# Optimization experiments

Measured on AMD Instinct MI355X. Metric: run time of the kernel, lower is better.

## Reference

```python
import jax, jax.numpy as jnp
import numpy as np

NUM_HEADS = 12
ROPE_THETA = 100.0

def _rotate_half(x):
    x1 = x[..., ::2]
    x2 = x[..., 1::2]
    return jnp.stack((-x2, x1), axis=-1).reshape(x.shape)

def _apply_rope(x, cos, sin):
    return x * cos + _rotate_half(x) * sin

def _rope_cos_sin(h, w, head_dim, theta):
    quarter = head_dim // 4  # head_dim=64 -> 16 freq bands
    inv_freq = 1.0 / theta ** (jnp.arange(quarter, dtype=jnp.float32) / max(quarter, 1))
    y = jnp.repeat(jnp.arange(h, dtype=jnp.float32), w)   # [h*w]
    xc = jnp.tile(jnp.arange(w, dtype=jnp.float32), h)    # [h*w]
    y_freqs = y[:, None] * inv_freq[None, :]               # [N, quarter]
    x_freqs = xc[:, None] * inv_freq[None, :]
    y_ang = jnp.repeat(y_freqs, 2, axis=-1)                # [N, half]
    x_ang = jnp.repeat(x_freqs, 2, axis=-1)
    ang = jnp.concatenate([y_ang, x_ang], axis=-1)         # [N, head_dim]
    return jnp.cos(ang)[None, None], jnp.sin(ang)[None, None]  # [1,1,N,hd]

def setup_inputs() -> dict:
    key = jax.random.key(0)
    ks = jax.random.split(key, 8)
    B, S, D = 8, 1025, 768
    s = 0.02
    return {
        "x": jax.random.normal(ks[0], (B, S, D), jnp.float32),
        "q_w": jax.random.normal(ks[1], (D, D), jnp.float32) * s,
        "q_b": jax.random.normal(ks[2], (D,), jnp.float32) * s,
        "k_w": jax.random.normal(ks[3], (D, D), jnp.float32) * s,
        "v_w": jax.random.normal(ks[4], (D, D), jnp.float32) * s,
        "v_b": jax.random.normal(ks[5], (D,), jnp.float32) * s,
        "o_w": jax.random.normal(ks[6], (D, D), jnp.float32) * s,
        "o_b": jax.random.normal(ks[7], (D,), jnp.float32) * s,
        "h": 32,
        "w": 32,
        "num_prefix_tokens": 1,
    }

def reference(x, q_w, q_b, k_w, v_w, v_b, o_w, o_b, h, w, num_prefix_tokens):
    B, S, D = x.shape
    H = NUM_HEADS
    hd = D // H
    scale = hd ** -0.5
    p = num_prefix_tokens

    def proj(W, b):
        y = jnp.einsum('bsd,ed->bse', x, W)
        if b is not None:
            y = y + b
        return y.reshape(B, S, H, hd).transpose(0, 2, 1, 3)  # [B,H,S,hd]

    q = proj(q_w, q_b)
    k = proj(k_w, None)
    v = proj(v_w, v_b)

    cos, sin = _rope_cos_sin(h, w, hd, ROPE_THETA)
    q = jnp.concatenate([q[:, :, :p], _apply_rope(q[:, :, p:], cos, sin)], axis=2)
    k = jnp.concatenate([k[:, :, :p], _apply_rope(k[:, :, p:], cos, sin)], axis=2)

    attn = jnp.einsum('bhqd,bhkd->bhqk', q * scale, k)
    attn = jax.nn.softmax(attn, axis=-1)
    out = jnp.einsum('bhqk,bhkd->bhqd', attn, v)
    out = out.transpose(0, 2, 1, 3).reshape(B, S, D)
    return jnp.einsum('bsd,ed->bse', out, o_w) + o_b
```

## Files before the change

### kernel.cpp

```cpp
#include <hip/hip_runtime.h>

typedef unsigned short u16;
typedef unsigned int   u32;
typedef __attribute__((ext_vector_type(4))) short s4;
typedef __attribute__((ext_vector_type(8))) short s8;
typedef __attribute__((ext_vector_type(4))) float f4;
typedef __attribute__((ext_vector_type(16))) float f16v;

#define NB   8
#define SEQ  1025
#define DIM  768
#define NH   12
#define HD   64
#define BPAD 1056
#define MPAD 8448
#define MV   8200
#define SQP  1056
#define SKP  1088
#define NG16 68
#define NQKV 2304
#define BHT  96
#define QSCALE 0.1803368801111204f

__device__ __forceinline__ u16 f2bf(float f) {
  u32 u = __builtin_bit_cast(u32, f);
  u += 0x7fffu + ((u >> 16) & 1u);
  return (u16)(u >> 16);
}
__device__ __forceinline__ float bf2f(u16 h) {
  return __builtin_bit_cast(float, ((u32)h) << 16);
}
__device__ __forceinline__ float exp2f_(float x) {
#if __has_builtin(__builtin_amdgcn_exp2f)
  return __builtin_amdgcn_exp2f(x);
#else
  return exp2f(x);
#endif
}
__device__ __forceinline__ u32 cvtpk(float a, float b) {
  u32 r;
  asm("v_cvt_pk_bf16_f32 %0, %1, %2" : "=v"(r) : "v"(a), "v"(b));
  return r;
}

typedef const __attribute__((address_space(1))) void cas1v;
typedef __attribute__((address_space(3))) void as3v;
__device__ __forceinline__ void gload16(const void* g, void* l) {
  __builtin_amdgcn_global_load_lds((cas1v*)g, (as3v*)l, 16, 0, 0);
}

#define MFMA16(a, b, c) __builtin_amdgcn_mfma_f32_16x16x32_bf16(a, b, c, 0, 0, 0)
#define MFMA32(a, b, c) __builtin_amdgcn_mfma_f32_32x32x16_bf16(a, b, c, 0, 0, 0)
#define BAR() __builtin_amdgcn_s_barrier()

__global__ void conv_x(const float* __restrict__ x, u16* __restrict__ xb) {
  int i = blockIdx.x * 256 + threadIdx.x;
  int e = i * 4;
  int row = e / DIM, col = e - row * DIM;
  int b = row / BPAD, s = row - b * BPAD;
  s4 o;
  if (s < SEQ) {
    float4 v = *(const float4*)(x + ((size_t)(b * SEQ + s)) * DIM + col);
    o[0] = (short)f2bf(v.x); o[1] = (short)f2bf(v.y);
    o[2] = (short)f2bf(v.z); o[3] = (short)f2bf(v.w);
  } else {
    o = (s4){0, 0, 0, 0};
  }
  *(s4*)(xb + e) = o;
}

__global__ void conv_w(const float* __restrict__ qw, const float* __restrict__ kw,
                       const float* __restrict__ vw, const float* __restrict__ ow,
                       const float* __restrict__ qb, const float* __restrict__ vb,
                       u16* __restrict__ wqkv, u16* __restrict__ wo, float* __restrict__ biasq,
                       float2* __restrict__ rt) {
  int i = blockIdx.x * 256 + threadIdx.x;
  wqkv[i]           = f2bf(qw[i]);
  wqkv[i + 589824]  = f2bf(kw[i]);
  wqkv[i + 1179648] = f2bf(vw[i]);
  wo[i]             = f2bf(ow[i]);
  if (i < NQKV) biasq[i] = (i < 768) ? qb[i] : (i < 1536 ? 0.f : vb[i - 1536]);
  if (i < SEQ * 32) {
    int s = i >> 5, jj = i & 31;
    float cs = 1.f, sn = 0.f;
    if (s > 0) {
      int tok = s - 1;
      int pos = (jj < 16) ? (tok >> 5) : (tok & 31);
      int f = jj & 15;
      float ang = (float)pos * __expf((float)f * -0.28782313662425572f);
      __sincosf(ang, &sn, &cs);
    }
    rt[i] = make_float2(cs, sn);
  }
}

__global__ __launch_bounds__(512, 2) void gemm_qkv(const u16* __restrict__ A, const u16* __restrict__ Bm,
                                                   const float* __restrict__ bias,
                                                   u16* __restrict__ Ql, u16* __restrict__ Kl,
                                                   u16* __restrict__ Vp, const float2* __restrict__ rt) {
  __shared__ u16 smem[73728];
  const int K = DIM;
  int tid = threadIdx.x;
  int lane = tid & 63, wave = tid >> 6;
  int g = lane >> 4, c16 = lane & 15;
  int wm = wave >> 1, wn = wave & 1;
  int nwg = gridDim.x, orig = blockIdx.x;
  int qd = nwg >> 3, rm = nwg & 7, xcd = orig & 7;
  int wgid = (xcd < rm ? xcd * (qd + 1) : rm * (qd + 1) + (xcd - rm) * qd) + (orig >> 3);
  int m0 = (wgid / 18) * 256, n0 = (wgid % 18) * 128;

  f4 acc[4][4] = {};

  int lr = lane >> 3;
  int lc = ((lane & 7) ^ lr) * 8;
  const u16* As0 = A  + (size_t)(m0 + wave * 8 + lr) * K + lc;
  const u16* Bs0 = Bm + (size_t)(n0 + wave * 8 + lr) * K + lc;

  auto stageA3 = [&](int sb, int ko) {
    u16* base = smem + sb * 24576 + wave * 512;
    gload16(As0 + ko,           base);
    gload16(As0 + 64 * K + ko,  base + 4096);
    gload16(As0 + 128 * K + ko, base + 8192);
  };
  auto stageB3 = [&](int sb, int ko) {
    u16* baseA = smem + sb * 24576 + wave * 512;
    u16* baseB = smem + sb * 24576 + 16384 + wave * 512;
    gload16(As0 + 192 * K + ko, baseA + 12288);
    gload16(Bs0 + ko,           baseB);
    gload16(Bs0 + 64 * K + ko,  baseB + 4096);
  };

  int rsw = (c16 & 7) << 3;
  int colk0 = (g * 8) ^ rsw;
  int colk1 = (g * 8 + 32) ^ rsw;

  stageA3(0, 0);  stageB3(0, 0);
  stageA3(1, 64); stageB3(1, 64);
  asm volatile("s_waitcnt vmcnt(6)" ::: "memory");
  BAR();

#pragma unroll 3
  for (int kt = 0; kt < 12; ++kt) {
    const u16* bp = smem + (kt % 3) * 24576;
    int sb = (kt + 2) % 3, ko = (kt + 2) * 64;
    bool st = kt < 10;
    s8 bfr[4][2], afr[2][2];
#pragma unroll
    for (int n = 0; n < 4; n++) {
      int rb = wn * 64 + n * 16 + c16;
      bfr[n][0] = *(const s8*)(bp + 16384 + rb * 64 + colk0);
      bfr[n][1] = *(const s8*)(bp + 16384 + rb * 64 + colk1);
    }
#pragma unroll
    for (int m = 0; m < 2; m++) {
      int ra = wm * 64 + m * 16 + c16;
      afr[m][0] = *(const s8*)(bp + ra * 64 + colk0);
      afr[m][1] = *(const s8*)(bp + ra * 64 + colk1);
    }
    if (st) stageA3(sb, ko);
    BAR();
    asm volatile("s_waitcnt lgkmcnt(0)" ::: "memory");
    __builtin_amdgcn_s_setprio(1);
#pragma unroll
    for (int m = 0; m < 2; m++)
#pragma unroll
      for (int n = 0; n < 4; n++) {
        acc[m][n] = MFMA16(afr[m][0], bfr[n][0], acc[m][n]);
        acc[m][n] = MFMA16(afr[m][1], bfr[n][1], acc[m][n]);
      }
    __builtin_amdgcn_s_setprio(0);
    BAR();
    s8 af2[2][2];
#pragma unroll
    for (int m = 0; m < 2; m++) {
      int ra = wm * 64 + (m + 2) * 16 + c16;
      af2[m][0] = *(const s8*)(bp + ra * 64 + colk0);
      af2[m][1] = *(const s8*)(bp + ra * 64 + colk1);
    }
    if (st) stageB3(sb, ko);
    BAR();
    asm volatile("s_waitcnt lgkmcnt(0)" ::: "memory");
    __builtin_amdgcn_s_setprio(1);
#pragma unroll
    for (int m = 0; m < 2; m++)
#pragma unroll
      for (int n = 0; n < 4; n++) {
        acc[m + 2][n] = MFMA16(af2[m][0], bfr[n][0], acc[m + 2][n]);
        acc[m + 2][n] = MFMA16(af2[m][1], bfr[n][1], acc[m + 2][n]);
      }
    __builtin_amdgcn_s_setprio(0);
    if (kt < 10)       asm volatile("s_waitcnt vmcnt(6)" ::: "memory");
    else if (kt == 10) asm volatile("s_waitcnt vmcnt(0)" ::: "memory");
    BAR();
  }

  __syncthreads();
  u16 (*ct)[130] = (u16(*)[130])smem;
  int part = (n0 >= 1536) ? 2 : (n0 >= 768 ? 1 : 0);
  float qs = (part == 0) ? QSCALE : 1.0f;
#pragma unroll
  for (int j = 0; j < 4; j++) {
    int col = wn * 64 + j * 16 + c16;
    float bv = bias[n0 + col];
    int jj = (col & 63) >> 1;
    int odd = col & 1;
#pragma unroll
    for (int i = 0; i < 4; i++) {
      int rowb = wm * 64 + i * 16 + g * 4;
#pragma unroll
      for (int r = 0; r < 4; r++) {
        float v = acc[i][j][r] + bv;
        u16 o;
        if (part < 2) {
          float vp = __shfl_xor(v, 1);
          int m = m0 + rowb + r;
          int s = m % BPAD;
          float2 t = rt[(s < SEQ ? s : SEQ - 1) * 32 + jj];
          float rv = odd ? (v * t.x + vp * t.y) : (v * t.x - vp * t.y);
          o = f2bf(rv * qs);
        } else {
          o = f2bf(v);
        }
        ct[rowb + r][col] = o;
      }
    }
  }
  __syncthreads();
  if (part < 2) {
    u16* dstB = (part == 0) ? Ql : Kl;
    int stride = (part == 0) ? SQP : SKP;
#pragma unroll
    for (int p = 0; p < 8; p++) {
      int task = p * 512 + tid;
      int row = task >> 4, cg = (task & 15) * 8;
      int m = m0 + row, b = m / BPAD, s = m - b * BPAD;
      int n = n0 + cg;
      int hq = (n >> 6) - part * NH;
      s8 v = *(const s8*)&ct[row][cg];
      *(s8*)(dstB + ((size_t)((b * NH + hq) * stride + s)) * HD + (n & 63)) = v;
    }
  } else {
#pragma unroll
    for (int p = 0; p < 4; p++) {
      int task = p * 512 + tid;
      int col = task & 127, rg = task >> 7;
      int mb = m0 + rg * 16, b = mb / BPAD, sb2 = mb - b * BPAD;
      int g16 = sb2 >> 4;
      int n = n0 + col;
      int hq = (n >> 6) - 2 * NH;
      s8 o0, o1;
#pragma unroll
      for (int k = 0; k < 16; k++) {
        int mp = (k & 3) | (((k >> 3) & 1) << 2) | (((k >> 2) & 1) << 3);
        u16 val = ct[rg * 16 + k][col];
        if (mp < 8) o0[mp] = (short)val; else o1[mp - 8] = (short)val;
      }
      u16* dst = Vp + ((size_t)((b * NH + hq) * NG16 + g16) * HD + (n & 63)) * 16;
      *(s8*)dst = o0;
      *(s8*)(dst + 8) = o1;
    }
  }
}

__global__ __launch_bounds__(256) void gemm_o(const u16* __restrict__ A, const u16* __restrict__ Bm,
                                              float* __restrict__ Cf, const float* __restrict__ bias,
                                              int N, int K, int Mvalid, int nnt) {
  __shared__ u16 smem[16384];
  int tid = threadIdx.x;
  int lane = tid & 63, wave = tid >> 6;
  int g = lane >> 4, c16 = lane & 15;
  int nwg = gridDim.x, orig = blockIdx.x;
  int qd = nwg >> 3, rm = nwg & 7, xcd = orig & 7;
  int wgid = (xcd < rm ? xcd * (qd + 1) : rm * (qd + 1) + (xcd - rm) * qd) + (orig >> 3);
  int m0 = (wgid / nnt) * 128, n0 = (wgid % nnt) * 128;
  int wm = wave >> 1, wn = wave & 1;
  f4 acc[4][4] = {};

  int ldrow = wave * 16 + (lane >> 2);
  int ldk = ((lane & 3) ^ ((ldrow >> 1) & 3)) * 8;
  const u16* Asrc = A + (size_t)(m0 + ldrow) * K + ldk;
  const u16* Bsrc = Bm + (size_t)(n0 + ldrow) * K + ldk;

  auto stage = [&](int buf, int k0) {
    u16* aw = smem + buf * 4096 + wave * 512;
    u16* bw = smem + 8192 + buf * 4096 + wave * 512;
    gload16(Asrc + k0, aw);
    gload16(Asrc + 64 * K + k0, aw + 2048);
    gload16(Bsrc + k0, bw);
    gload16(Bsrc + 64 * K + k0, bw + 2048);
  };

  stage(0, 0);
  __syncthreads();
  int nk = K >> 5;
  int kx = (g ^ ((c16 >> 1) & 3)) * 8;
  for (int t = 0; t < nk; t++) {
    int buf = t & 1;
    if (t + 1 < nk) stage(buf ^ 1, (t + 1) << 5);
    s8 af[4], bf[4];
#pragma unroll
    for (int i = 0; i < 4; i++) {
      af[i] = *(const s8*)(smem + buf * 4096 + (wm * 64 + i * 16 + c16) * 32 + kx);
      bf[i] = *(const s8*)(smem + 8192 + buf * 4096 + (wn * 64 + i * 16 + c16) * 32 + kx);
    }
    __builtin_amdgcn_s_setprio(1);
#pragma unroll
    for (int i = 0; i < 4; i++)
#pragma unroll
      for (int j = 0; j < 4; j++)
        acc[i][j] = MFMA16(af[i], bf[j], acc[i][j]);
    __builtin_amdgcn_s_setprio(0);
    __syncthreads();
  }

#pragma unroll
  for (int i = 0; i < 4; i++)
#pragma unroll
    for (int j = 0; j < 4; j++) {
      int n = n0 + wn * 64 + j * 16 + c16;
      float bv = bias[n];
#pragma unroll
      for (int r = 0; r < 4; r++) {
        int m = m0 + wm * 64 + i * 16 + g * 4 + r;
        if (m < Mvalid) Cf[(size_t)m * N + n] = acc[i][j][r] + bv;
      }
    }
}

__global__ __launch_bounds__(256) void attn_k(const u16* __restrict__ Q, const u16* __restrict__ K,
                                              const u16* __restrict__ Vp, u16* __restrict__ Ao) {
  __shared__ u16 lds[2][2][64 * 64];
  int bh = blockIdx.x;
  int tid = threadIdx.x;
  int wave = tid >> 6, lane = tid & 63;
  int q32 = lane & 31, h = lane >> 5;
  int b = bh / NH, hh = bh % NH;
  int qb = blockIdx.y * 128 + wave * 32;
  if (qb > SEQ - 32) qb = SEQ - 32;
  const u16* Qb = Q + (size_t)bh * SQP * HD;
  const u16* Kb = K + (size_t)bh * SKP * HD;
  const u16* Vb = Vp + (size_t)bh * NG16 * 1024;

  s8 qf[4];
#pragma unroll
  for (int t = 0; t < 4; t++)
    qf[t] = *(const s8*)(Qb + (size_t)(qb + q32) * HD + 16 * t + 8 * h);

  f16v o0 = {}, o1 = {};
  float mrun = -3e38f, lrun = 0.f;
  int swz = (q32 & 7) << 4;

  auto stage = [&](int buf, int c) {
#pragma unroll
    for (int i = 0; i < 2; i++) {
      int sb = i * 4096 + tid * 16;
      int row = sb >> 7;
      int ch = (sb >> 4) & 7;
      int so = (ch ^ (row & 7)) * 8;
      u16* kd = &lds[buf][0][i * 2048 + wave * 512];
      u16* vd = &lds[buf][1][i * 2048 + wave * 512];
      gload16(Kb + (size_t)(c * 64 + row) * HD + so, kd);
      gload16(Vb + c * 4096 + i * 2048 + tid * 8, vd);
    }
  };

  stage(0, 0);
  __syncthreads();

  for (int c = 0; c < 17; c++) {
    int buf = c & 1;
    if (c < 16) stage(buf ^ 1, c + 1);
    const char* Ks = (const char*)&lds[buf][0][0];
    const char* Vs = (const char*)&lds[buf][1][0];

    f16v st0 = {}, st1 = {};
    __builtin_amdgcn_s_setprio(1);
#pragma unroll
    for (int t = 0; t < 4; t++) {
      int off = (32 * t + 16 * h) ^ swz;
      s8 a0 = *(const s8*)(Ks + q32 * 128 + off);
      s8 a1 = *(const s8*)(Ks + (32 + q32) * 128 + off);
      st0 = MFMA32(a0, qf[t], st0);
      st1 = MFMA32(a1, qf[t], st1);
    }
    __builtin_amdgcn_s_setprio(0);

    s8 vf0[4], vf1[4];
#pragma unroll
    for (int s = 0; s < 4; s++) {
      vf0[s] = *(const s8*)(Vs + 2048 * s + 32 * q32 + 16 * h);
      vf1[s] = *(const s8*)(Vs + 2048 * s + 1024 + 32 * q32 + 16 * h);
    }

    if (c == 16) {
      st0[0] = h ? -3e38f : st0[0];
#pragma unroll
      for (int r = 1; r < 16; r++) st0[r] = -3e38f;
#pragma unroll
      for (int r = 0; r < 16; r++) st1[r] = -3e38f;
    }

    float mx[8];
#pragma unroll
    for (int r = 0; r < 8; r++)
      mx[r] = fmaxf(fmaxf(st0[r], st0[r + 8]), fmaxf(st1[r], st1[r + 8]));
#pragma unroll
    for (int w = 4; w >= 1; w >>= 1)
#pragma unroll
      for (int r = 0; r < w; r++) mx[r] = fmaxf(mx[r], mx[r + w]);
    float pmax = fmaxf(mx[0], __shfl_xor(mx[0], 32));

    if (!__all(pmax <= mrun + 11.5f)) {
      float mnew = fmaxf(mrun, pmax);
      float cf = exp2f_(mrun - mnew);
      lrun *= cf;
      mrun = mnew;
#pragma unroll
      for (int r = 0; r < 16; r++) {
        float c2 = __shfl(cf, (r & 3) + 8 * (r >> 2) + 4 * h);
        o0[r] *= c2;
        o1[r] *= c2;
      }
    }

    float sm[8];
#pragma unroll
    for (int r = 0; r < 16; r++) {
      st0[r] = exp2f_(st0[r] - mrun);
      st1[r] = exp2f_(st1[r] - mrun);
    }
#pragma unroll
    for (int r = 0; r < 8; r++) sm[r] = (st0[r] + st0[r + 8]) + (st1[r] + st1[r + 8]);
#pragma unroll
    for (int w = 4; w >= 1; w >>= 1)
#pragma unroll
      for (int r = 0; r < w; r++) sm[r] += sm[r + w];
    lrun += sm[0] + __shfl_xor(sm[0], 32);

    __builtin_amdgcn_s_setprio(1);
#pragma unroll
    for (int s = 0; s < 4; s++) {
      union { s8 v; u32 w[4]; } pa;
#pragma unroll
      for (int i = 0; i < 4; i++) {
        float plo = (s < 2) ? st0[8 * (s & 1) + 2 * i]     : st1[8 * (s & 1) + 2 * i];
        float phi = (s < 2) ? st0[8 * (s & 1) + 2 * i + 1] : st1[8 * (s & 1) + 2 * i + 1];
        pa.w[i] = cvtpk(plo, phi);
      }
      o0 = MFMA32(pa.v, vf0[s], o0);
      o1 = MFMA32(pa.v, vf1[s], o1);
    }
    __builtin_amdgcn_s_setprio(0);
    __syncthreads();
  }

  float rl = 1.0f / lrun;
#pragma unroll
  for (int r = 0; r < 16; r++) {
    int cr = (r & 3) + 8 * (r >> 2) + 4 * h;
    float sc = __shfl(rl, cr);
    u16* dst = Ao + (size_t)(b * SEQ + qb + cr) * DIM + hh * HD;
    dst[q32]      = f2bf(o0[r] * sc);
    dst[32 + q32] = f2bf(o1[r] * sc);
  }
}

extern "C" void kernel_launch(void* const* d_in, const int* in_sizes, int n_in,
                              void* d_out, int out_size, void* d_ws, size_t ws_size,
                              hipStream_t stream) {
  const float* x  = (const float*)d_in[0];
  const float* qw = (const float*)d_in[1];
  const float* qb = (const float*)d_in[2];
  const float* kw = (const float*)d_in[3];
  const float* vw = (const float*)d_in[4];
  const float* vb = (const float*)d_in[5];
  const float* ow = (const float*)d_in[6];
  const float* ob = (const float*)d_in[7];
  float* out = (float*)d_out;

  char* ws = (char*)d_ws;
  u16*    xb   = (u16*)(ws);
  u16*    wqkv = (u16*)(ws + 12976128);
  u16*    wo   = (u16*)(ws + 16515072);
  float*  bq   = (float*)(ws + 17694720);
  float2* rt   = (float2*)(ws + 17703936);
  u16*    Ql   = (u16*)(ws + 17966336);
  u16*    Kl   = (u16*)(ws + 30942464);
  u16*    Vp   = (u16*)(ws + 44311808);
  u16*    Ao   = xb;

  conv_x<<<6336, 256, 0, stream>>>(x, xb);
  conv_w<<<2304, 256, 0, stream>>>(qw, kw, vw, ow, qb, vb, wqkv, wo, bq, rt);
  gemm_qkv<<<594, 512, 0, stream>>>(xb, wqkv, bq, Ql, Kl, Vp, rt);
  attn_k<<<dim3(96, 9), 256, 0, stream>>>(Ql, Kl, Vp, Ao);
  gemm_o<<<390, 256, 0, stream>>>(Ao, wo, out, ob, DIM, DIM, MV, 6);
}
```

Baseline: 161.4 us.

## Enlarge QKV GEMM tile to 256x256 with double-buffered LDS and 2x4 waves

The fused QKV projection GEMM now uses 256x256 output tiles instead of 256x128. Each of 8 waves computes 128x64, and K tiles are double-buffered instead of triple-buffered, which halves the grid to 297 blocks at one block per CU. The larger tile is meant to raise operand reuse and cut global and LDS traffic per FLOP. In exchange, 297 blocks on 256 CUs leaves a ragged tail wave, occupancy drops, and there is less load-latency hiding.

```diff
diff --git a/kernel.cpp b/kernel.cpp
--- a/kernel.cpp
+++ b/kernel.cpp
@@ -52,6 +52,7 @@
 #define MFMA16(a, b, c) __builtin_amdgcn_mfma_f32_16x16x32_bf16(a, b, c, 0, 0, 0)
 #define MFMA32(a, b, c) __builtin_amdgcn_mfma_f32_32x32x16_bf16(a, b, c, 0, 0, 0)
 #define BAR() __builtin_amdgcn_s_barrier()
+#define LGKM0() do { asm volatile("s_waitcnt lgkmcnt(0)" ::: "memory"); __builtin_amdgcn_sched_barrier(0); } while (0)
 
 __global__ void conv_x(const float* __restrict__ x, u16* __restrict__ xb) {
   int i = blockIdx.x * 256 + threadIdx.x;
@@ -94,108 +95,143 @@
   }
 }
 
-__global__ __launch_bounds__(512, 2) void gemm_qkv(const u16* __restrict__ A, const u16* __restrict__ Bm,
+__global__ __launch_bounds__(512, 1) void gemm_qkv(const u16* __restrict__ A, const u16* __restrict__ Bm,
                                                    const float* __restrict__ bias,
                                                    u16* __restrict__ Ql, u16* __restrict__ Kl,
                                                    u16* __restrict__ Vp, const float2* __restrict__ rt) {
-  __shared__ u16 smem[73728];
+  __shared__ u16 smem[66560];
   const int K = DIM;
   int tid = threadIdx.x;
   int lane = tid & 63, wave = tid >> 6;
   int g = lane >> 4, c16 = lane & 15;
-  int wm = wave >> 1, wn = wave & 1;
+  int wm = wave >> 2, wn = wave & 3;
   int nwg = gridDim.x, orig = blockIdx.x;
   int qd = nwg >> 3, rm = nwg & 7, xcd = orig & 7;
   int wgid = (xcd < rm ? xcd * (qd + 1) : rm * (qd + 1) + (xcd - rm) * qd) + (orig >> 3);
-  int m0 = (wgid / 18) * 256, n0 = (wgid % 18) * 128;
-
-  f4 acc[4][4] = {};
-
-  int lr = lane >> 3;
-  int lc = ((lane & 7) ^ lr) * 8;
-  const u16* As0 = A  + (size_t)(m0 + wave * 8 + lr) * K + lc;
-  const u16* Bs0 = Bm + (size_t)(n0 + wave * 8 + lr) * K + lc;
-
-  auto stageA3 = [&](int sb, int ko) {
-    u16* base = smem + sb * 24576 + wave * 512;
-    gload16(As0 + ko,           base);
-    gload16(As0 + 64 * K + ko,  base + 4096);
-    gload16(As0 + 128 * K + ko, base + 8192);
+  int m0 = (wgid / 9) * 256, n0 = (wgid % 9) * 256;
+
+  f4 acc[8][4] = {};
+
+  int lr = lane >> 3, lc8 = lane & 7;
+  int scol = (lc8 ^ lr) * 8;
+  int rh = wave * 16 + lr;
+  const u16* As0 = A  + (size_t)(m0 + rh) * K + scol;
+  const u16* Bs0 = Bm + (size_t)(n0 + rh) * K + scol;
+
+  auto stageA = [&](int buf, int ko) {
+    u16* d = smem + buf * 32768 + wave * 1024;
+    gload16(As0 + ko,            d);
+    gload16(As0 + 8 * K + ko,    d + 512);
+    gload16(As0 + 128 * K + ko,  d + 8192);
+    gload16(As0 + 136 * K + ko,  d + 8192 + 512);
   };
-  auto stageB3 = [&](int sb, int ko) {
-    u16* baseA = smem + sb * 24576 + wave * 512;
-    u16* baseB = smem + sb * 24576 + 16384 + wave * 512;
-    gload16(As0 + 192 * K + ko, baseA + 12288);
-    gload16(Bs0 + ko,           baseB);
-    gload16(Bs0 + 64 * K + ko,  baseB + 4096);
+  auto stageB = [&](int buf, int ko) {
+    u16* d = smem + buf * 32768 + 16384 + wave * 1024;
+    gload16(Bs0 + ko,            d);
+    gload16(Bs0 + 8 * K + ko,    d + 512);
+    gload16(Bs0 + 128 * K + ko,  d + 8192);
+    gload16(Bs0 + 136 * K + ko,  d + 8192 + 512);
   };
 
-  int rsw = (c16 & 7) << 3;
-  int colk0 = (g * 8) ^ rsw;
-  int colk1 = (g * 8 + 32) ^ rsw;
-
-  stageA3(0, 0);  stageB3(0, 0);
-  stageA3(1, 64); stageB3(1, 64);
-  asm volatile("s_waitcnt vmcnt(6)" ::: "memory");
+  int bc0 = (g * 16) ^ ((c16 & 7) << 4);
+  int bc1 = (64 + g * 16) ^ ((c16 & 7) << 4);
+  int rowB = wn * 64 + c16;
+
+  stageA(0, 0); stageB(0, 0);
+  asm volatile("s_waitcnt vmcnt(0)" ::: "memory");
   BAR();
 
-#pragma unroll 3
-  for (int kt = 0; kt < 12; ++kt) {
-    const u16* bp = smem + (kt % 3) * 24576;
-    int sb = (kt + 2) % 3, ko = (kt + 2) * 64;
-    bool st = kt < 10;
-    s8 bfr[4][2], afr[2][2];
-#pragma unroll
-    for (int n = 0; n < 4; n++) {
-      int rb = wn * 64 + n * 16 + c16;
-      bfr[n][0] = *(const s8*)(bp + 16384 + rb * 64 + colk0);
-      bfr[n][1] = *(const s8*)(bp + 16384 + rb * 64 + colk1);
-    }
-#pragma unroll
-    for (int m = 0; m < 2; m++) {
-      int ra = wm * 64 + m * 16 + c16;
-      afr[m][0] = *(const s8*)(bp + ra * 64 + colk0);
-      afr[m][1] = *(const s8*)(bp + ra * 64 + colk1);
-    }
-    if (st) stageA3(sb, ko);
-    BAR();
-    asm volatile("s_waitcnt lgkmcnt(0)" ::: "memory");
-    __builtin_amdgcn_s_setprio(1);
-#pragma unroll
-    for (int m = 0; m < 2; m++)
-#pragma unroll
-      for (int n = 0; n < 4; n++) {
-        acc[m][n] = MFMA16(afr[m][0], bfr[n][0], acc[m][n]);
-        acc[m][n] = MFMA16(afr[m][1], bfr[n][1], acc[m][n]);
-      }
-    __builtin_amdgcn_s_setprio(0);
-    BAR();
-    s8 af2[2][2];
-#pragma unroll
-    for (int m = 0; m < 2; m++) {
-      int ra = wm * 64 + (m + 2) * 16 + c16;
-      af2[m][0] = *(const s8*)(bp + ra * 64 + colk0);
-      af2[m][1] = *(const s8*)(bp + ra * 64 + colk1);
-    }
-    if (st) stageB3(sb, ko);
-    BAR();
-    asm volatile("s_waitcnt lgkmcnt(0)" ::: "memory");
-    __builtin_amdgcn_s_setprio(1);
-#pragma unroll
-    for (int m = 0; m < 2; m++)
-#pragma unroll
-      for (int n = 0; n < 4; n++) {
-        acc[m + 2][n] = MFMA16(af2[m][0], bfr[n][0], acc[m + 2][n]);
-        acc[m + 2][n] = MFMA16(af2[m][1], bfr[n][1], acc[m + 2][n]);
-      }
-    __builtin_amdgcn_s_setprio(0);
-    if (kt < 10)       asm volatile("s_waitcnt vmcnt(6)" ::: "memory");
-    else if (kt == 10) asm volatile("s_waitcnt vmcnt(0)" ::: "memory");
+#pragma unroll 2
+  for (int t = 0; t < 12; ++t) {
+    const char* bp = (const char*)smem + (t & 1) * 65536;
+    int ko = (t + 1) * 64;
+    bool st = t < 11;
+    s8 bf[4][2], af[2][2];
+#pragma unroll
+    for (int j = 0; j < 4; j++) {
+      const char* rb = bp + 32768 + (rowB + j * 16) * 128;
+      bf[j][0] = *(const s8*)(rb + bc0);
+      bf[j][1] = *(const s8*)(rb + bc1);
+    }
+#pragma unroll
+    for (int i = 0; i < 2; i++) {
+      const char* ra = bp + (wm * 128 + i * 16 + c16) * 128;
+      af[i][0] = *(const s8*)(ra + bc0);
+      af[i][1] = *(const s8*)(ra + bc1);
+    }
+    if (st) stageA((t & 1) ^ 1, ko);
+    BAR();
+    LGKM0();
+    __builtin_amdgcn_s_setprio(1);
+#pragma unroll
+    for (int i = 0; i < 2; i++)
+#pragma unroll
+      for (int j = 0; j < 4; j++) {
+        acc[i][j] = MFMA16(af[i][0], bf[j][0], acc[i][j]);
+        acc[i][j] = MFMA16(af[i][1], bf[j][1], acc[i][j]);
+      }
+    __builtin_amdgcn_s_setprio(0);
+    BAR();
+#pragma unroll
+    for (int i = 0; i < 2; i++) {
+      const char* ra = bp + (wm * 128 + (i + 2) * 16 + c16) * 128;
+      af[i][0] = *(const s8*)(ra + bc0);
+      af[i][1] = *(const s8*)(ra + bc1);
+    }
+    if (st) stageB((t & 1) ^ 1, ko);
+    BAR();
+    LGKM0();
+    __builtin_amdgcn_s_setprio(1);
+#pragma unroll
+    for (int i = 0; i < 2; i++)
+#pragma unroll
+      for (int j = 0; j < 4; j++) {
+        acc[i + 2][j] = MFMA16(af[i][0], bf[j][0], acc[i + 2][j]);
+        acc[i + 2][j] = MFMA16(af[i][1], bf[j][1], acc[i + 2][j]);
+      }
+    __builtin_amdgcn_s_setprio(0);
+    BAR();
+#pragma unroll
+    for (int i = 0; i < 2; i++) {
+      const char* ra = bp + (wm * 128 + (i + 4) * 16 + c16) * 128;
+      af[i][0] = *(const s8*)(ra + bc0);
+      af[i][1] = *(const s8*)(ra + bc1);
+    }
+    BAR();
+    LGKM0();
+    __builtin_amdgcn_s_setprio(1);
+#pragma unroll
+    for (int i = 0; i < 2; i++)
+#pragma unroll
+      for (int j = 0; j < 4; j++) {
+        acc[i + 4][j] = MFMA16(af[i][0], bf[j][0], acc[i + 4][j]);
+        acc[i + 4][j] = MFMA16(af[i][1], bf[j][1], acc[i + 4][j]);
+      }
+    __builtin_amdgcn_s_setprio(0);
+    BAR();
+#pragma unroll
+    for (int i = 0; i < 2; i++) {
+      const char* ra = bp + (wm * 128 + (i + 6) * 16 + c16) * 128;
+      af[i][0] = *(const s8*)(ra + bc0);
+      af[i][1] = *(const s8*)(ra + bc1);
+    }
+    BAR();
+    LGKM0();
+    __builtin_amdgcn_s_setprio(1);
+#pragma unroll
+    for (int i = 0; i < 2; i++)
+#pragma unroll
+      for (int j = 0; j < 4; j++) {
+        acc[i + 6][j] = MFMA16(af[i][0], bf[j][0], acc[i + 6][j]);
+        acc[i + 6][j] = MFMA16(af[i][1], bf[j][1], acc[i + 6][j]);
+      }
+    __builtin_amdgcn_s_setprio(0);
+    if (st) asm volatile("s_waitcnt vmcnt(0)" ::: "memory");
     BAR();
   }
 
   __syncthreads();
-  u16 (*ct)[130] = (u16(*)[130])smem;
+  u16 (*ct)[258] = (u16(*)[258])smem;
   int part = (n0 >= 1536) ? 2 : (n0 >= 768 ? 1 : 0);
   float qs = (part == 0) ? QSCALE : 1.0f;
 #pragma unroll
@@ -205,8 +241,8 @@
     int jj = (col & 63) >> 1;
     int odd = col & 1;
 #pragma unroll
-    for (int i = 0; i < 4; i++) {
-      int rowb = wm * 64 + i * 16 + g * 4;
+    for (int i = 0; i < 8; i++) {
+      int rowb = wm * 128 + i * 16 + g * 4;
 #pragma unroll
       for (int r = 0; r < 4; r++) {
         float v = acc[i][j][r] + bv;
@@ -215,8 +251,8 @@
           float vp = __shfl_xor(v, 1);
           int m = m0 + rowb + r;
           int s = m % BPAD;
-          float2 t = rt[(s < SEQ ? s : SEQ - 1) * 32 + jj];
-          float rv = odd ? (v * t.x + vp * t.y) : (v * t.x - vp * t.y);
+          float2 tt = rt[(s < SEQ ? s : SEQ - 1) * 32 + jj];
+          float rv = odd ? (v * tt.x + vp * tt.y) : (v * tt.x - vp * tt.y);
           o = f2bf(rv * qs);
         } else {
           o = f2bf(v);
@@ -230,9 +266,9 @@
     u16* dstB = (part == 0) ? Ql : Kl;
     int stride = (part == 0) ? SQP : SKP;
 #pragma unroll
-    for (int p = 0; p < 8; p++) {
+    for (int p = 0; p < 16; p++) {
       int task = p * 512 + tid;
-      int row = task >> 4, cg = (task & 15) * 8;
+      int row = task >> 5, cg = (task & 31) * 8;
       int m = m0 + row, b = m / BPAD, s = m - b * BPAD;
       int n = n0 + cg;
       int hq = (n >> 6) - part * NH;
@@ -241,9 +277,9 @@
     }
   } else {
 #pragma unroll
-    for (int p = 0; p < 4; p++) {
+    for (int p = 0; p < 8; p++) {
       int task = p * 512 + tid;
-      int col = task & 127, rg = task >> 7;
+      int col = task & 255, rg = task >> 8;
       int mb = m0 + rg * 16, b = mb / BPAD, sb2 = mb - b * BPAD;
       int g16 = sb2 >> 4;
       int n = n0 + col;
@@ -491,7 +527,7 @@
 
   conv_x<<<6336, 256, 0, stream>>>(x, xb);
   conv_w<<<2304, 256, 0, stream>>>(qw, kw, vw, ow, qb, vb, wqkv, wo, bq, rt);
-  gemm_qkv<<<594, 512, 0, stream>>>(xb, wqkv, bq, Ql, Kl, Vp, rt);
+  gemm_qkv<<<297, 512, 0, stream>>>(xb, wqkv, bq, Ql, Kl, Vp, rt);
   attn_k<<<dim3(96, 9), 256, 0, stream>>>(Ql, Kl, Vp, Ao);
   gemm_o<<<390, 256, 0, stream>>>(Ao, wo, out, ob, DIM, DIM, MV, 6);
 }
```

Result: no change. 163.8 us (+1.5%).
